# Performance work log

Measured on AMD Instinct MI355X. Metric: run time of the kernel, lower is better.

Reference implementation:

```python
import jax, jax.numpy as jnp
import numpy as np

D = 1024
HEADS = 16
HEAD_DIM = D // HEADS
EPS = 1e-5


def layer_norm(x, gamma, beta):
    mu = jnp.mean(x, axis=-1, keepdims=True)
    var = jnp.mean(jnp.square(x - mu), axis=-1, keepdims=True)
    return (x - mu) * jax.lax.rsqrt(var + EPS) * gamma + beta


def setup_inputs() -> dict:
    key = jax.random.key(0)
    ks = jax.random.split(key, 8)
    B, S = 4, 2048
    s_in = 1.0 / np.sqrt(D)
    s_ffn = 1.0 / np.sqrt(4 * D)
    return {
        "x": jax.random.normal(ks[0], (B, S, D), dtype=jnp.float32),
        "ln1_g": jnp.ones((D,), jnp.float32),
        "ln1_b": jnp.zeros((D,), jnp.float32),
        "w_qkv": jax.random.uniform(ks[1], (D, 3 * D), jnp.float32, -s_in, s_in),
        "b_qkv": jnp.zeros((3 * D,), jnp.float32),
        "w_out": jax.random.uniform(ks[2], (D, D), jnp.float32, -s_in, s_in),
        "b_out": jnp.zeros((D,), jnp.float32),
        "ln2_g": jnp.ones((D,), jnp.float32),
        "ln2_b": jnp.zeros((D,), jnp.float32),
        "w_ffn1": jax.random.uniform(ks[3], (D, 4 * D), jnp.float32, -s_in, s_in),
        "b_ffn1": jnp.zeros((4 * D,), jnp.float32),
        "w_ffn2": jax.random.uniform(ks[4], (4 * D, D), jnp.float32, -s_ffn, s_ffn),
        "b_ffn2": jnp.zeros((D,), jnp.float32),
    }


def reference(x, ln1_g, ln1_b, w_qkv, b_qkv, w_out, b_out,
              ln2_g, ln2_b, w_ffn1, b_ffn1, w_ffn2, b_ffn2):
    B, S, Dm = x.shape
    h = layer_norm(x, ln1_g, ln1_b)
    qkv = h @ w_qkv + b_qkv  # [B,S,3D]
    q, k, v = jnp.split(qkv, 3, axis=-1)
    # [B,S,D] -> [B,H,S,hd]
    def to_heads(t):
        return t.reshape(B, S, HEADS, HEAD_DIM).transpose(0, 2, 1, 3)
    q, k, v = to_heads(q), to_heads(k), to_heads(v)
    scores = jnp.einsum('bhqd,bhkd->bhqk', q, k) / np.sqrt(HEAD_DIM).astype(np.float32)
    attn = jax.nn.softmax(scores, axis=-1)
    out = jnp.einsum('bhqk,bhkd->bhqd', attn, v)
    out = out.transpose(0, 2, 1, 3).reshape(B, S, Dm)
    x = x + (out @ w_out + b_out)
    h = layer_norm(x, ln2_g, ln2_b)
    h = jax.nn.gelu(h @ w_ffn1 + b_ffn1, approximate=False) @ w_ffn2 + b_ffn2
    return x + h
```

## Files before the change

### kernel.cpp

```cpp
#include <hip/hip_runtime.h>
#include <cstdint>
#include <cstddef>

typedef unsigned short u16;
typedef unsigned int   u32;
typedef __bf16 bf16x8 __attribute__((ext_vector_type(8)));
typedef float  f32x4  __attribute__((ext_vector_type(4)));
static_assert(sizeof(bf16x8) == 16, "bf16x8 must be 16B");
static_assert(sizeof(f32x4) == 16, "f32x4 must be 16B");

#define DEVI static __device__ __forceinline__

#define QSCALE 0.18033688011112042f

DEVI float fexp2(float x) {
  float r;
  asm("v_exp_f32 %0, %1" : "=v"(r) : "v"(x));
  return r;
}

DEVI u16 f2bf(float x) {
  u32 u = __builtin_bit_cast(u32, x);
  u = (u + 0x7FFFu + ((u >> 16) & 1u)) >> 16;
  return (u16)u;
}

DEVI void gload16(const u16* g, u16* l) {
  __builtin_amdgcn_global_load_lds(
      (const __attribute__((address_space(1))) void*)g,
      (__attribute__((address_space(3))) void*)l, 16, 0, 0);
}

#define S_BARRIER() asm volatile("s_barrier" ::: "memory")
#define VMCNT(n) asm volatile("s_waitcnt vmcnt(" #n ")" ::: "memory")

template <int MO, int NACC>
DEVI void mm16(f32x4 (&acc)[NACC][4], const bf16x8 (&af)[4], const bf16x8 (&bf)[4]) {
  __builtin_amdgcn_s_setprio(1);
#pragma unroll
  for (int m = 0; m < 4; m++)
#pragma unroll
    for (int n = 0; n < 4; n++)
      acc[MO + m][n] =
          __builtin_amdgcn_mfma_f32_16x16x32_bf16(af[m], bf[n], acc[MO + m][n], 0, 0, 0);
  __builtin_amdgcn_s_setprio(0);
}

__global__ __launch_bounds__(256) void transpose_cvt(const float* __restrict__ W,
                                                     u16* __restrict__ WT,
                                                     int K, int N,
                                                     float scale, int nscale) {
  __shared__ float tile[32][33];
  int tx = threadIdx.x & 31, ty = threadIdx.x >> 5;
  int c0 = blockIdx.x * 32, r0 = blockIdx.y * 32;
#pragma unroll
  for (int i = 0; i < 4; i++)
    tile[ty + i * 8][tx] = W[(size_t)(r0 + ty + i * 8) * N + c0 + tx];
  __syncthreads();
#pragma unroll
  for (int i = 0; i < 4; i++) {
    int r = ty + i * 8;
    int n = c0 + r;
    float scl = (n < nscale) ? scale : 1.f;
    WT[(size_t)n * K + r0 + tx] = f2bf(tile[tx][r] * scl);
  }
}

__global__ __launch_bounds__(256) void prep_bias(const float* __restrict__ b,
                                                 float* __restrict__ o) {
  int i = blockIdx.x * 256 + threadIdx.x;
  o[i] = b[i] * (i < 1024 ? QSCALE : 1.f);
}

__global__ __launch_bounds__(256) void ln_k(const float* __restrict__ X,
                                            const float* __restrict__ gam,
                                            const float* __restrict__ bet,
                                            u16* __restrict__ H) {
  __shared__ float2 part[4];
  int row = blockIdx.x, t = threadIdx.x;
  const float4* xr = (const float4*)(X + (size_t)row * 1024);
  float4 v = xr[t];
  float s = v.x + v.y + v.z + v.w;
  float q = v.x * v.x + v.y * v.y + v.z * v.z + v.w * v.w;
#pragma unroll
  for (int o = 32; o > 0; o >>= 1) {
    s += __shfl_xor(s, o);
    q += __shfl_xor(q, o);
  }
  if ((t & 63) == 0) part[t >> 6] = make_float2(s, q);
  __syncthreads();
  float S = part[0].x + part[1].x + part[2].x + part[3].x;
  float Q = part[0].y + part[1].y + part[2].y + part[3].y;
  float mu = S * (1.f / 1024.f);
  float rs = rsqrtf(Q * (1.f / 1024.f) - mu * mu + 1e-5f);
  float4 gv = ((const float4*)gam)[t];
  float4 bv = ((const float4*)bet)[t];
  ushort4 o;
  o.x = f2bf((v.x - mu) * rs * gv.x + bv.x);
  o.y = f2bf((v.y - mu) * rs * gv.y + bv.y);
  o.z = f2bf((v.z - mu) * rs * gv.z + bv.z);
  o.w = f2bf((v.w - mu) * rs * gv.w + bv.w);
  *(ushort4*)(H + (size_t)row * 1024 + t * 4) = o;
}

template <int EPI, int NACC>
DEVI void epilogue(f32x4 (&acc)[NACC][4], const float* bias, const float* res,
                   float* outF, u16* outB, int N, int rbase, int cbase, int g, int li) {
#pragma unroll
  for (int n = 0; n < 4; n++) {
    int c = cbase + n * 16 + li;
    float bv = bias[c];
#pragma unroll
    for (int a = 0; a < NACC; a++) {
      int rowb = rbase + a * 16 + g * 4;
#pragma unroll
      for (int r = 0; r < 4; r++) {
        size_t idx = (size_t)(rowb + r) * N + c;
        float v = acc[a][n][r] + bv;
        if constexpr (EPI == 1) {
          v += res[idx];
          outF[idx] = v;
        } else if constexpr (EPI == 2) {
          float te = fminf(v * (2.3020246f + 0.10294562f * v * v), 80.f);
          float e = fexp2(te);
          float rc;
          asm("v_rcp_f32 %0, %1" : "=v"(rc) : "v"(e + 1.f));
          v = v * e * rc;
          outB[idx] = f2bf(v);
        } else {
          outB[idx] = f2bf(v);
        }
      }
    }
  }
}

template <int EPI>
__global__ __launch_bounds__(1024, 4) void gemm256(const u16* __restrict__ A,
                                                   const u16* __restrict__ Bt,
                                                   const float* __restrict__ bias,
                                                   const float* __restrict__ res,
                                                   float* __restrict__ outF,
                                                   u16* __restrict__ outB,
                                                   int M, int N, int K) {
  __shared__ uint4 As[2][2048];
  __shared__ uint4 Bs[2][2048];
  const int t = threadIdx.x, lane = t & 63, wv = t >> 6;
  const int wr = wv >> 2, wc = wv & 3;
  const int li = lane & 15, g = lane >> 4;

  const int gx = gridDim.x;
  const int nwg = gx * gridDim.y;
  const int wg = blockIdx.y * gx + blockIdx.x;
  const int swz = (wg & 7) * (nwg >> 3) + (wg >> 3);
  const int bx = swz % gx, by = swz / gx;
  const int bm0 = by * 256, bn0 = bx * 256;

  f32x4 acc[4][4];
  const f32x4 z4 = {0.f, 0.f, 0.f, 0.f};
#pragma unroll
  for (int a = 0; a < 4; a++)
#pragma unroll
    for (int n = 0; n < 4; n++) acc[a][n] = z4;

  const u16* aB = A + (size_t)(bm0 + wv * 16 + li) * K + g * 8;
  const u16* bB = Bt + (size_t)(bn0 + wv * 16 + li) * K + g * 8;

  auto stA = [&](int buf, int kh, int kt) {
    gload16(aB + (size_t)kt * 64 + kh * 32, (u16*)&As[buf][(kh * 16 + wv) * 64]);
  };
  auto stB = [&](int buf, int kh, int kt) {
    gload16(bB + (size_t)kt * 64 + kh * 32, (u16*)&Bs[buf][(kh * 16 + wv) * 64]);
  };

  stA(0, 0, 0); stB(0, 0, 0);
  stA(0, 1, 0); stB(0, 1, 0);
  VMCNT(2);
  S_BARRIER();

  const int NT = K >> 6;
  int cur = 0;
  for (int kt = 0; kt < NT; kt++) {
    const int nx = cur ^ 1;
    const bool more = (kt + 1 < NT);
    bf16x8 af[4], bf[4];
#pragma unroll
    for (int n = 0; n < 4; n++)
      bf[n] = __builtin_bit_cast(bf16x8, Bs[cur][(wc * 4 + n) * 64 + lane]);
#pragma unroll
    for (int m = 0; m < 4; m++)
      af[m] = __builtin_bit_cast(bf16x8, As[cur][(wr * 4 + m) * 64 + lane]);
    if (more) { stA(nx, 0, kt + 1); stB(nx, 0, kt + 1); }
    S_BARRIER();
    mm16<0>(acc, af, bf);
    if (more) { VMCNT(2); } else { VMCNT(0); }
    S_BARRIER();
#pragma unroll
    for (int n = 0; n < 4; n++)
      bf[n] = __builtin_bit_cast(bf16x8, Bs[cur][(16 + wc * 4 + n) * 64 + lane]);
#pragma unroll
    for (int m = 0; m < 4; m++)
      af[m] = __builtin_bit_cast(bf16x8, As[cur][(16 + wr * 4 + m) * 64 + lane]);
    if (more) { stA(nx, 1, kt + 1); stB(nx, 1, kt + 1); }
    S_BARRIER();
    mm16<0>(acc, af, bf);
    if (more) { VMCNT(2); }
    S_BARRIER();
    cur = nx;
  }

  epilogue<EPI>(acc, bias, res, outF, outB, N, bm0 + wr * 64, bn0 + wc * 64, g, li);
}

template <int EPI>
__global__ __launch_bounds__(512, 1) void gemm128(const u16* __restrict__ A,
                                                  const u16* __restrict__ Bt,
                                                  const float* __restrict__ bias,
                                                  const float* __restrict__ res,
                                                  float* __restrict__ outF,
                                                  u16* __restrict__ outB,
                                                  int M, int N, int K) {
  __shared__ uint4 As[2][1024];
  __shared__ uint4 Bs[2][2048];
  const int t = threadIdx.x, lane = t & 63, wv = t >> 6;
  const int wr = wv >> 2, wc = wv & 3;
  const int li = lane & 15, g = lane >> 4;

  const int gx = gridDim.x;
  const int nwg = gx * gridDim.y;
  const int wg = blockIdx.y * gx + blockIdx.x;
  const int swz = (wg & 7) * (nwg >> 3) + (wg >> 3);
  const int bx = swz % gx, by = swz / gx;
  const int bm0 = by * 128, bn0 = bx * 256;

  f32x4 acc[4][4];
  const f32x4 z4 = {0.f, 0.f, 0.f, 0.f};
#pragma unroll
  for (int a = 0; a < 4; a++)
#pragma unroll
    for (int n = 0; n < 4; n++) acc[a][n] = z4;

  const u16* aB = A + (size_t)(bm0 + wv * 16 + li) * K + g * 8;
  const u16* bB = Bt + (size_t)(bn0 + wv * 16 + li) * K + g * 8;
  const size_t rskip = (size_t)128 * K;

  auto stA = [&](int buf, int j, int kt) {
    gload16(aB + (size_t)kt * 64 + j * 32, (u16*)&As[buf][(j * 8 + wv) * 64]);
  };
  auto stB = [&](int buf, int j, int kt) {
    gload16(bB + (size_t)kt * 64 + ((j & 1) ? rskip : (size_t)0) + (j >> 1) * 32,
            (u16*)&Bs[buf][(j * 8 + wv) * 64]);
  };

  stA(0, 0, 0); stB(0, 0, 0); stB(0, 1, 0);
  stA(0, 1, 0); stB(0, 2, 0); stB(0, 3, 0);
  VMCNT(3);
  S_BARRIER();

  const int NT = K >> 6;
  int cur = 0;
  for (int kt = 0; kt < NT; kt++) {
    const int nx = cur ^ 1;
    const bool more = (kt + 1 < NT);
    bf16x8 af[4], bf[4];
#pragma unroll
    for (int n = 0; n < 4; n++)
      bf[n] = __builtin_bit_cast(bf16x8, Bs[cur][(wc * 4 + n) * 64 + lane]);
#pragma unroll
    for (int m = 0; m < 4; m++)
      af[m] = __builtin_bit_cast(bf16x8, As[cur][(wr * 4 + m) * 64 + lane]);
    if (more) { stA(nx, 0, kt + 1); stB(nx, 0, kt + 1); stB(nx, 1, kt + 1); }
    S_BARRIER();
    mm16<0>(acc, af, bf);
    if (more) { VMCNT(3); } else { VMCNT(0); }
    S_BARRIER();
#pragma unroll
    for (int n = 0; n < 4; n++)
      bf[n] = __builtin_bit_cast(bf16x8, Bs[cur][(16 + wc * 4 + n) * 64 + lane]);
#pragma unroll
    for (int m = 0; m < 4; m++)
      af[m] = __builtin_bit_cast(bf16x8, As[cur][(8 + wr * 4 + m) * 64 + lane]);
    if (more) { stA(nx, 1, kt + 1); stB(nx, 2, kt + 1); stB(nx, 3, kt + 1); }
    S_BARRIER();
    mm16<0>(acc, af, bf);
    if (more) { VMCNT(3); }
    S_BARRIER();
    cur = nx;
  }

  epilogue<EPI>(acc, bias, res, outF, outB, N, bm0 + wr * 64, bn0 + wc * 64, g, li);
}

__global__ __launch_bounds__(256) void v_tr(const u16* __restrict__ qkv,
                                            u16* __restrict__ vfm) {
  __shared__ u16 Vl[64 * 72];
  const int t = threadIdx.x;
  const int bh = blockIdx.y;
  const int bb = bh >> 4, h = bh & 15;
  const int kt = blockIdx.x;
#pragma unroll
  for (int bq = 0; bq < 2; bq++) {
    int c = t + bq * 256;
    int key = c >> 3, d0 = (c & 7) * 8;
    uint4 v = *(const uint4*)(qkv + (size_t)(bb * 2048 + kt * 64 + key) * 3072 + 2048 +
                              h * 64 + d0);
    *(uint4*)&Vl[key * 72 + d0] = v;
  }
  __syncthreads();
#pragma unroll
  for (int bq = 0; bq < 2; bq++) {
    int oc = t + bq * 256;
    int f = oc >> 6, l = oc & 63;
    int db = f >> 1, g32 = f & 1;
    int li = l & 15, g = l >> 4;
    u16 tmp[8];
#pragma unroll
    for (int e = 0; e < 8; e++) {
      int pk = g32 * 32 + ((e & 4) << 2) + g * 4 + (e & 3);
      tmp[e] = Vl[pk * 72 + db * 16 + li];
    }
    *(uint4*)(vfm + ((((size_t)bh * 32 + kt) * 8 + f) * 64 + l) * 8) = *(uint4*)tmp;
  }
}

__global__ __launch_bounds__(256) void attn_k(const u16* __restrict__ qkv,
                                              const u16* __restrict__ vfm,
                                              u16* __restrict__ ao) {
  __shared__ uint4 Ks[512];
  __shared__ uint4 Vs[512];
  const int t = threadIdx.x, lane = t & 63, wv = t >> 6;
  const int g = lane >> 4, li = lane & 15;
  const int bb = blockIdx.y >> 4, h = blockIdx.y & 15;
  const int q0 = blockIdx.x * 64 + wv * 16;

  const size_t qoff = (size_t)(bb * 2048 + q0 + li) * 3072 + h * 64 + g * 8;
  bf16x8 qf0 = __builtin_bit_cast(bf16x8, *(const uint4*)(qkv + qoff));
  bf16x8 qf1 = __builtin_bit_cast(bf16x8, *(const uint4*)(qkv + qoff + 32));

  const u16* kbase = qkv + (size_t)bb * 2048 * 3072 + 1024 + h * 64;
  const int f1 = wv + 4;
  const u16* ksrc0 = kbase + (size_t)(((wv >> 1) << 4) + li) * 3072 + ((wv & 1) << 5) + g * 8;
  const u16* ksrc1 = kbase + (size_t)(((f1 >> 1) << 4) + li) * 3072 + ((f1 & 1) << 5) + g * 8;
  const u16* vsrc0 = vfm + ((size_t)(bb * 16 + h) * 32) * 4096 + (wv * 64 + lane) * 8;
  const u16* vsrc1 = vsrc0 + 4 * 64 * 8;

  const f32x4 z4 = {0.f, 0.f, 0.f, 0.f};
  f32x4 Of[4];
#pragma unroll
  for (int db = 0; db < 4; db++) Of[db] = z4;
  f32x4 Ol = z4;

  bf16x8 vone;
#pragma unroll
  for (int j = 0; j < 8; j++) vone[j] = (__bf16)1.0f;

  for (int tile = 0; tile < 32; tile++) {
    __syncthreads();
    gload16(ksrc0 + (size_t)tile * 64 * 3072, (u16*)&Ks[wv * 64]);
    gload16(ksrc1 + (size_t)tile * 64 * 3072, (u16*)&Ks[(wv + 4) * 64]);
    gload16(vsrc0 + (size_t)tile * 4096, (u16*)&Vs[wv * 64]);
    gload16(vsrc1 + (size_t)tile * 4096, (u16*)&Vs[(wv + 4) * 64]);
    __syncthreads();

#pragma unroll
    for (int g32 = 0; g32 < 2; g32++) {
      uint4 pw;
#pragma unroll
      for (int tt = 0; tt < 2; tt++) {
        int kb16 = g32 * 2 + tt;
        bf16x8 k0f = __builtin_bit_cast(bf16x8, Ks[(kb16 * 2 + 0) * 64 + lane]);
        bf16x8 k1f = __builtin_bit_cast(bf16x8, Ks[(kb16 * 2 + 1) * 64 + lane]);
        f32x4 st = z4;
        st = __builtin_amdgcn_mfma_f32_16x16x32_bf16(k0f, qf0, st, 0, 0, 0);
        st = __builtin_amdgcn_mfma_f32_16x16x32_bf16(k1f, qf1, st, 0, 0, 0);
        float e0 = fexp2(st[0]), e1 = fexp2(st[1]);
        float e2 = fexp2(st[2]), e3 = fexp2(st[3]);
        u32 wa, wb;
        asm("v_cvt_pk_bf16_f32 %0, %1, %2" : "=v"(wa) : "v"(e0), "v"(e1));
        asm("v_cvt_pk_bf16_f32 %0, %1, %2" : "=v"(wb) : "v"(e2), "v"(e3));
        if (tt == 0) { pw.x = wa; pw.y = wb; }
        else         { pw.z = wa; pw.w = wb; }
      }
      bf16x8 pf = __builtin_bit_cast(bf16x8, pw);
      __builtin_amdgcn_s_setprio(1);
#pragma unroll
      for (int db = 0; db < 4; db++) {
        bf16x8 vf = __builtin_bit_cast(bf16x8, Vs[(db * 2 + g32) * 64 + lane]);
        Of[db] = __builtin_amdgcn_mfma_f32_16x16x32_bf16(pf, vf, Of[db], 0, 0, 0);
      }
      Ol = __builtin_amdgcn_mfma_f32_16x16x32_bf16(pf, vone, Ol, 0, 0, 0);
      __builtin_amdgcn_s_setprio(0);
    }
  }

  float invl[4];
#pragma unroll
  for (int r = 0; r < 4; r++) invl[r] = 1.f / Ol[r];
#pragma unroll
  for (int db = 0; db < 4; db++)
#pragma unroll
    for (int r = 0; r < 4; r++)
      ao[(size_t)(bb * 2048 + q0 + 4 * g + r) * 1024 + h * 64 + db * 16 + li] =
          f2bf(Of[db][r] * invl[r]);
}

extern "C" void kernel_launch(void* const* d_in, const int* in_sizes, int n_in,
                              void* d_out, int out_size, void* d_ws, size_t ws_size,
                              hipStream_t stream) {
  const float* x = (const float*)d_in[0];
  const float* ln1g = (const float*)d_in[1];
  const float* ln1b = (const float*)d_in[2];
  const float* wqkv = (const float*)d_in[3];
  const float* bqkv = (const float*)d_in[4];
  const float* wout = (const float*)d_in[5];
  const float* bout = (const float*)d_in[6];
  const float* ln2g = (const float*)d_in[7];
  const float* ln2b = (const float*)d_in[8];
  const float* wff1 = (const float*)d_in[9];
  const float* bff1 = (const float*)d_in[10];
  const float* wff2 = (const float*)d_in[11];
  const float* bff2 = (const float*)d_in[12];
  float* outF = (float*)d_out;
  char* ws = (char*)d_ws;

  u16* wqkvT = (u16*)(ws + 0);
  u16* woutT = (u16*)(ws + 6291456);
  u16* wff1T = (u16*)(ws + 8388608);
  u16* wff2T = (u16*)(ws + 16777216);
  u16* hbuf  = (u16*)(ws + 25165824);
  u16* vfm   = (u16*)(ws + 25165824);
  u16* qkvb  = (u16*)(ws + 41943040);
  u16* attnb = (u16*)(ws + 92274688);
  u16* ffn1b = qkvb;
  float* biasq = (float*)attnb;

  transpose_cvt<<<dim3(96, 32), 256, 0, stream>>>(wqkv, wqkvT, 1024, 3072, QSCALE, 1024);
  transpose_cvt<<<dim3(32, 32), 256, 0, stream>>>(wout, woutT, 1024, 1024, 1.f, 0);
  transpose_cvt<<<dim3(128, 32), 256, 0, stream>>>(wff1, wff1T, 1024, 4096, 1.f, 0);
  transpose_cvt<<<dim3(32, 128), 256, 0, stream>>>(wff2, wff2T, 4096, 1024, 1.f, 0);
  prep_bias<<<12, 256, 0, stream>>>(bqkv, biasq);

  ln_k<<<8192, 256, 0, stream>>>(x, ln1g, ln1b, hbuf);
  gemm128<0><<<dim3(12, 64), 512, 0, stream>>>(hbuf, wqkvT, biasq, nullptr, nullptr, qkvb,
                                               8192, 3072, 1024);
  v_tr<<<dim3(32, 64), 256, 0, stream>>>(qkvb, vfm);
  attn_k<<<dim3(32, 64), 256, 0, stream>>>(qkvb, vfm, attnb);
  gemm128<1><<<dim3(4, 64), 512, 0, stream>>>(attnb, woutT, bout, x, outF, nullptr,
                                              8192, 1024, 1024);
  ln_k<<<8192, 256, 0, stream>>>(outF, ln2g, ln2b, hbuf);
  gemm256<2><<<dim3(16, 32), 1024, 0, stream>>>(hbuf, wff1T, bff1, nullptr, nullptr, ffn1b,
                                                8192, 4096, 1024);
  gemm128<1><<<dim3(4, 64), 512, 0, stream>>>(ffn1b, wff2T, bff2, outF, outF, nullptr,
                                              8192, 1024, 4096);

  (void)in_sizes;
  (void)n_in;
  (void)out_size;
  (void)ws_size;
}
```

Measured before the change: 446.3 us.

## Shrink gemm128 K-tile with prefetch-two pipeline and double Q rows per attention wave

The 128x256 GEMM now works on 32-wide K slices with smaller LDS buffers. It keeps two stages in flight and issues the prefetch after the MFMAs, and raises the launch-bounds occupancy hint to allow more resident workgroups. The attention kernel now has each wave process 32 query rows instead of 16, so every loaded K/V tile is reused across two query blocks, and the grid is halved. The attention change doubles accumulator registers and cuts the number of workgroups. The GEMM change adds more barriers per unit of K work.

```diff
diff --git a/kernel.cpp b/kernel.cpp
--- a/kernel.cpp
+++ b/kernel.cpp
@@ -213,15 +213,15 @@
 }
 
 template <int EPI>
-__global__ __launch_bounds__(512, 1) void gemm128(const u16* __restrict__ A,
+__global__ __launch_bounds__(512, 6) void gemm128(const u16* __restrict__ A,
                                                   const u16* __restrict__ Bt,
                                                   const float* __restrict__ bias,
                                                   const float* __restrict__ res,
                                                   float* __restrict__ outF,
                                                   u16* __restrict__ outB,
                                                   int M, int N, int K) {
-  __shared__ uint4 As[2][1024];
-  __shared__ uint4 Bs[2][2048];
+  __shared__ uint4 As[2][512];
+  __shared__ uint4 Bs[2][1024];
   const int t = threadIdx.x, lane = t & 63, wv = t >> 6;
   const int wr = wv >> 2, wc = wv & 3;
   const int li = lane & 15, g = lane >> 4;
@@ -240,28 +240,25 @@
 #pragma unroll
     for (int n = 0; n < 4; n++) acc[a][n] = z4;
 
-  const u16* aB = A + (size_t)(bm0 + wv * 16 + li) * K + g * 8;
-  const u16* bB = Bt + (size_t)(bn0 + wv * 16 + li) * K + g * 8;
-  const size_t rskip = (size_t)128 * K;
-
-  auto stA = [&](int buf, int j, int kt) {
-    gload16(aB + (size_t)kt * 64 + j * 32, (u16*)&As[buf][(j * 8 + wv) * 64]);
+  const u16* aS = A + (size_t)(bm0 + wv * 16 + li) * K + g * 8;
+  const u16* bS0 = Bt + (size_t)(bn0 + wv * 16 + li) * K + g * 8;
+  const u16* bS1 = Bt + (size_t)(bn0 + (8 + wv) * 16 + li) * K + g * 8;
+
+  auto stage = [&](int buf, int kt) {
+    const size_t ko = (size_t)kt * 32;
+    gload16(aS + ko, (u16*)&As[buf][wv * 64]);
+    gload16(bS0 + ko, (u16*)&Bs[buf][wv * 64]);
+    gload16(bS1 + ko, (u16*)&Bs[buf][(8 + wv) * 64]);
   };
-  auto stB = [&](int buf, int j, int kt) {
-    gload16(bB + (size_t)kt * 64 + ((j & 1) ? rskip : (size_t)0) + (j >> 1) * 32,
-            (u16*)&Bs[buf][(j * 8 + wv) * 64]);
-  };
-
-  stA(0, 0, 0); stB(0, 0, 0); stB(0, 1, 0);
-  stA(0, 1, 0); stB(0, 2, 0); stB(0, 3, 0);
+
+  stage(0, 0);
+  stage(1, 1);
   VMCNT(3);
   S_BARRIER();
 
-  const int NT = K >> 6;
+  const int NT = K >> 5;
   int cur = 0;
   for (int kt = 0; kt < NT; kt++) {
-    const int nx = cur ^ 1;
-    const bool more = (kt + 1 < NT);
     bf16x8 af[4], bf[4];
 #pragma unroll
     for (int n = 0; n < 4; n++)
@@ -269,23 +266,17 @@
 #pragma unroll
     for (int m = 0; m < 4; m++)
       af[m] = __builtin_bit_cast(bf16x8, As[cur][(wr * 4 + m) * 64 + lane]);
-    if (more) { stA(nx, 0, kt + 1); stB(nx, 0, kt + 1); stB(nx, 1, kt + 1); }
+    mm16<0>(acc, af, bf);
     S_BARRIER();
-    mm16<0>(acc, af, bf);
-    if (more) { VMCNT(3); } else { VMCNT(0); }
-    S_BARRIER();
-#pragma unroll
-    for (int n = 0; n < 4; n++)
-      bf[n] = __builtin_bit_cast(bf16x8, Bs[cur][(16 + wc * 4 + n) * 64 + lane]);
-#pragma unroll
-    for (int m = 0; m < 4; m++)
-      af[m] = __builtin_bit_cast(bf16x8, As[cur][(8 + wr * 4 + m) * 64 + lane]);
-    if (more) { stA(nx, 1, kt + 1); stB(nx, 2, kt + 1); stB(nx, 3, kt + 1); }
-    S_BARRIER();
-    mm16<0>(acc, af, bf);
-    if (more) { VMCNT(3); }
-    S_BARRIER();
-    cur = nx;
+    if (kt + 2 < NT) {
+      stage(cur, kt + 2);
+      VMCNT(3);
+      S_BARRIER();
+    } else if (kt + 1 < NT) {
+      VMCNT(0);
+      S_BARRIER();
+    }
+    cur ^= 1;
   }
 
   epilogue<EPI>(acc, bias, res, outF, outB, N, bm0 + wr * 64, bn0 + wc * 64, g, li);
@@ -331,11 +322,14 @@
   const int t = threadIdx.x, lane = t & 63, wv = t >> 6;
   const int g = lane >> 4, li = lane & 15;
   const int bb = blockIdx.y >> 4, h = blockIdx.y & 15;
-  const int q0 = blockIdx.x * 64 + wv * 16;
-
-  const size_t qoff = (size_t)(bb * 2048 + q0 + li) * 3072 + h * 64 + g * 8;
-  bf16x8 qf0 = __builtin_bit_cast(bf16x8, *(const uint4*)(qkv + qoff));
-  bf16x8 qf1 = __builtin_bit_cast(bf16x8, *(const uint4*)(qkv + qoff + 32));
+  const int q0 = blockIdx.x * 128 + wv * 32;
+
+  const size_t qoff0 = (size_t)(bb * 2048 + q0 + li) * 3072 + h * 64 + g * 8;
+  const size_t qoff1 = (size_t)(bb * 2048 + q0 + 16 + li) * 3072 + h * 64 + g * 8;
+  bf16x8 qf00 = __builtin_bit_cast(bf16x8, *(const uint4*)(qkv + qoff0));
+  bf16x8 qf01 = __builtin_bit_cast(bf16x8, *(const uint4*)(qkv + qoff0 + 32));
+  bf16x8 qf10 = __builtin_bit_cast(bf16x8, *(const uint4*)(qkv + qoff1));
+  bf16x8 qf11 = __builtin_bit_cast(bf16x8, *(const uint4*)(qkv + qoff1 + 32));
 
   const u16* kbase = qkv + (size_t)bb * 2048 * 3072 + 1024 + h * 64;
   const int f1 = wv + 4;
@@ -345,10 +339,10 @@
   const u16* vsrc1 = vsrc0 + 4 * 64 * 8;
 
   const f32x4 z4 = {0.f, 0.f, 0.f, 0.f};
-  f32x4 Of[4];
-#pragma unroll
-  for (int db = 0; db < 4; db++) Of[db] = z4;
-  f32x4 Ol = z4;
+  f32x4 Of0[4], Of1[4];
+#pragma unroll
+  for (int db = 0; db < 4; db++) { Of0[db] = z4; Of1[db] = z4; }
+  f32x4 Ol0 = z4, Ol1 = z4;
 
   bf16x8 vone;
 #pragma unroll
@@ -364,44 +358,54 @@
 
 #pragma unroll
     for (int g32 = 0; g32 < 2; g32++) {
-      uint4 pw;
+      uint4 pw0, pw1;
 #pragma unroll
       for (int tt = 0; tt < 2; tt++) {
         int kb16 = g32 * 2 + tt;
         bf16x8 k0f = __builtin_bit_cast(bf16x8, Ks[(kb16 * 2 + 0) * 64 + lane]);
         bf16x8 k1f = __builtin_bit_cast(bf16x8, Ks[(kb16 * 2 + 1) * 64 + lane]);
-        f32x4 st = z4;
-        st = __builtin_amdgcn_mfma_f32_16x16x32_bf16(k0f, qf0, st, 0, 0, 0);
-        st = __builtin_amdgcn_mfma_f32_16x16x32_bf16(k1f, qf1, st, 0, 0, 0);
-        float e0 = fexp2(st[0]), e1 = fexp2(st[1]);
-        float e2 = fexp2(st[2]), e3 = fexp2(st[3]);
-        u32 wa, wb;
-        asm("v_cvt_pk_bf16_f32 %0, %1, %2" : "=v"(wa) : "v"(e0), "v"(e1));
-        asm("v_cvt_pk_bf16_f32 %0, %1, %2" : "=v"(wb) : "v"(e2), "v"(e3));
-        if (tt == 0) { pw.x = wa; pw.y = wb; }
-        else         { pw.z = wa; pw.w = wb; }
+        f32x4 s0 = z4, s1 = z4;
+        s0 = __builtin_amdgcn_mfma_f32_16x16x32_bf16(k0f, qf00, s0, 0, 0, 0);
+        s0 = __builtin_amdgcn_mfma_f32_16x16x32_bf16(k1f, qf01, s0, 0, 0, 0);
+        s1 = __builtin_amdgcn_mfma_f32_16x16x32_bf16(k0f, qf10, s1, 0, 0, 0);
+        s1 = __builtin_amdgcn_mfma_f32_16x16x32_bf16(k1f, qf11, s1, 0, 0, 0);
+        float a0 = fexp2(s0[0]), a1 = fexp2(s0[1]), a2 = fexp2(s0[2]), a3 = fexp2(s0[3]);
+        float b0 = fexp2(s1[0]), b1 = fexp2(s1[1]), b2 = fexp2(s1[2]), b3 = fexp2(s1[3]);
+        u32 wa0, wa1, wb0, wb1;
+        asm("v_cvt_pk_bf16_f32 %0, %1, %2" : "=v"(wa0) : "v"(a0), "v"(a1));
+        asm("v_cvt_pk_bf16_f32 %0, %1, %2" : "=v"(wa1) : "v"(a2), "v"(a3));
+        asm("v_cvt_pk_bf16_f32 %0, %1, %2" : "=v"(wb0) : "v"(b0), "v"(b1));
+        asm("v_cvt_pk_bf16_f32 %0, %1, %2" : "=v"(wb1) : "v"(b2), "v"(b3));
+        if (tt == 0) { pw0.x = wa0; pw0.y = wa1; pw1.x = wb0; pw1.y = wb1; }
+        else         { pw0.z = wa0; pw0.w = wa1; pw1.z = wb0; pw1.w = wb1; }
       }
-      bf16x8 pf = __builtin_bit_cast(bf16x8, pw);
+      bf16x8 pfa = __builtin_bit_cast(bf16x8, pw0);
+      bf16x8 pfb = __builtin_bit_cast(bf16x8, pw1);
       __builtin_amdgcn_s_setprio(1);
 #pragma unroll
       for (int db = 0; db < 4; db++) {
         bf16x8 vf = __builtin_bit_cast(bf16x8, Vs[(db * 2 + g32) * 64 + lane]);
-        Of[db] = __builtin_amdgcn_mfma_f32_16x16x32_bf16(pf, vf, Of[db], 0, 0, 0);
+        Of0[db] = __builtin_amdgcn_mfma_f32_16x16x32_bf16(pfa, vf, Of0[db], 0, 0, 0);
+        Of1[db] = __builtin_amdgcn_mfma_f32_16x16x32_bf16(pfb, vf, Of1[db], 0, 0, 0);
       }
-      Ol = __builtin_amdgcn_mfma_f32_16x16x32_bf16(pf, vone, Ol, 0, 0, 0);
+      Ol0 = __builtin_amdgcn_mfma_f32_16x16x32_bf16(pfa, vone, Ol0, 0, 0, 0);
+      Ol1 = __builtin_amdgcn_mfma_f32_16x16x32_bf16(pfb, vone, Ol1, 0, 0, 0);
       __builtin_amdgcn_s_setprio(0);
     }
   }
 
-  float invl[4];
-#pragma unroll
-  for (int r = 0; r < 4; r++) invl[r] = 1.f / Ol[r];
+  float inv0[4], inv1[4];
+#pragma unroll
+  for (int r = 0; r < 4; r++) { inv0[r] = 1.f / Ol0[r]; inv1[r] = 1.f / Ol1[r]; }
 #pragma unroll
   for (int db = 0; db < 4; db++)
 #pragma unroll
-    for (int r = 0; r < 4; r++)
+    for (int r = 0; r < 4; r++) {
       ao[(size_t)(bb * 2048 + q0 + 4 * g + r) * 1024 + h * 64 + db * 16 + li] =
-          f2bf(Of[db][r] * invl[r]);
+          f2bf(Of0[db][r] * inv0[r]);
+      ao[(size_t)(bb * 2048 + q0 + 16 + 4 * g + r) * 1024 + h * 64 + db * 16 + li] =
+          f2bf(Of1[db][r] * inv1[r]);
+    }
 }
 
 extern "C" void kernel_launch(void* const* d_in, const int* in_sizes, int n_in,
@@ -444,7 +448,7 @@
   gemm128<0><<<dim3(12, 64), 512, 0, stream>>>(hbuf, wqkvT, biasq, nullptr, nullptr, qkvb,
                                                8192, 3072, 1024);
   v_tr<<<dim3(32, 64), 256, 0, stream>>>(qkvb, vfm);
-  attn_k<<<dim3(32, 64), 256, 0, stream>>>(qkvb, vfm, attnb);
+  attn_k<<<dim3(16, 64), 256, 0, stream>>>(qkvb, vfm, attnb);
   gemm128<1><<<dim3(4, 64), 512, 0, stream>>>(attnb, woutT, bout, x, outF, nullptr,
                                               8192, 1024, 1024);
   ln_k<<<8192, 256, 0, stream>>>(outF, ln2g, ln2b, hbuf);
```

Measured after the change: 1.512 ms. 3.39x slower.
